# Performance work log

Measured on AMD Instinct MI355X. Metric: run time of the kernel, lower is better.

The kernel has to match this reference:

```python
import jax, jax.numpy as jnp
import numpy as np

B, LQ, LK = 4, 2048, 2048
DQ, DK, DO = 1024, 1024, 1024


def setup_inputs() -> dict:
    key = jax.random.key(0)
    ks = jax.random.split(key, 9)
    s = 0.02
    return {
        "query_input": jax.random.normal(ks[0], (B, LQ, DQ), jnp.float32),
        "key_input": jax.random.normal(ks[1], (B, LK, DK), jnp.float32),
        "value_input": jax.random.normal(ks[2], (B, LK, DK), jnp.float32),
        "Wq": jax.random.normal(ks[3], (DQ, DO), jnp.float32) * s,
        "bq": jax.random.normal(ks[4], (DO,), jnp.float32) * s,
        "Wk": jax.random.normal(ks[5], (DK, DO), jnp.float32) * s,
        "bk": jax.random.normal(ks[6], (DO,), jnp.float32) * s,
        "Wv": jax.random.normal(ks[7], (DK, DO), jnp.float32) * s,
        "bv": jax.random.normal(ks[8], (DO,), jnp.float32) * s,
    }


def reference(query_input, key_input, value_input, Wq, bq, Wk, bk, Wv, bv):
    scale = jnp.asarray(DO, query_input.dtype) ** 0.5
    q = query_input @ Wq + bq              # [B, Lq, D]
    k = key_input @ Wk + bk                # [B, Lk, D]
    v = value_input @ Wv + bv              # [B, Lk, D]
    attn = jnp.einsum("bqd,bkd->bqk", q, k) / scale
    attn = jax.nn.softmax(attn, axis=-1)
    return jnp.einsum("bqk,bkd->bqd", attn, v)
```

## Files before the change

### kernel.cpp

```cpp
#include <hip/hip_runtime.h>

typedef _Float16 f16x8 __attribute__((ext_vector_type(8)));
typedef _Float16 f16x4 __attribute__((ext_vector_type(4)));
typedef float f32x4 __attribute__((ext_vector_type(4)));

__device__ __forceinline__ void lds_load16(const _Float16* g, _Float16* l) {
    __builtin_amdgcn_global_load_lds(
        (const __attribute__((address_space(1))) void*)g,
        (__attribute__((address_space(3))) void*)l,
        16, 0, 0);
}

template <int MODE>
__global__ __launch_bounds__(256, 4)
void gemm_core(const _Float16* A, const _Float16* B, void* Cv, const float* bias,
               const _Float16* Ax1, const _Float16* Bx1, void* Cx1, const float* bx1,
               const _Float16* Ax2, const _Float16* Bx2, void* Cx2, const float* bx2,
               float* rowsum)
{
    const int z = blockIdx.z;
    const int bx = blockIdx.x, by = blockIdx.y;
    size_t cbase = 0;
    int lda, ldb, K, m0, n0;
    if (MODE == 0) {
        const int tmy = bx * 8 + (by >> 3);
        const int tnx = by & 7;
        if (z == 1) { A = Ax1; B = Bx1; Cv = Cx1; bias = bx1; }
        else if (z == 2) { A = Ax2; B = Bx2; Cv = Cx2; bias = bx2; }
        lda = 1024; ldb = 1024; K = 1024;
        m0 = (z == 2 ? tnx : tmy) * 128;
        n0 = (z == 2 ? tmy : tnx) * 128;
    } else if (MODE == 3) {
        const int tm = (bx & 7) * 2 + (by >> 3);
        const int tn = (bx >> 3) * 8 + (by & 7);
        A += (size_t)z * 2048 * 1024;
        B += (size_t)z * 2048 * 1024;
        cbase = (size_t)z * 2048 * 2048;
        rowsum += z * 2048;
        lda = 1024; ldb = 1024; K = 1024;
        m0 = tm * 128; n0 = tn * 128;
    } else {
        const int tm = bx * 2 + (by >> 3);
        const int tn = by & 7;
        A += (size_t)z * 2048 * 2048;
        B += (size_t)z * 2048;
        cbase = (size_t)z * 2048 * 1024;
        rowsum += z * 2048;
        lda = 2048; ldb = 8192; K = 2048;
        m0 = tm * 128; n0 = tn * 128;
    }

    __shared__ __align__(16) _Float16 As[2][128 * 32];
    __shared__ __align__(16) _Float16 Bs[2][128 * 32];

    const int t    = threadIdx.x;
    const int w    = t >> 6;
    const int lane = t & 63;
    const int ln   = lane & 15;
    const int kq   = lane >> 4;
    const int wm   = (w & 1) * 64;
    const int wn   = (w >> 1) * 64;

    const int arow = t >> 2;
    const int kcf  = (t & 3) * 8;
    const _Float16* gA0 = A + (size_t)(m0 + arow) * lda + kcf;
    const _Float16* gA1 = A + (size_t)(m0 + 64 + arow) * lda + kcf;
    const _Float16* gB0 = B + (size_t)(n0 + arow) * ldb + kcf;
    const _Float16* gB1 = B + (size_t)(n0 + 64 + arow) * ldb + kcf;

    auto stage = [&](int buf, int k0) {
        lds_load16(gA0 + k0, As[buf] + w * 512);
        lds_load16(gA1 + k0, As[buf] + 2048 + w * 512);
        lds_load16(gB0 + k0, Bs[buf] + w * 512);
        lds_load16(gB1 + k0, Bs[buf] + 2048 + w * 512);
    };

    f32x4 acc[4][4] = {};

    stage(0, 0);
    int cur = 0;
#pragma unroll 2
    for (int k0 = 0; k0 < K; k0 += 32) {
        __syncthreads();
        if (k0 + 32 < K) stage(cur ^ 1, k0 + 32);

        const _Float16* Ab = As[cur];
        const _Float16* Bb = Bs[cur];
        f16x8 af[4], bf[4];
#pragma unroll
        for (int i = 0; i < 4; ++i)
            af[i] = *(const f16x8*)(Ab + (wm + i * 16 + ln) * 32 + kq * 8);
#pragma unroll
        for (int i = 0; i < 4; ++i)
            bf[i] = *(const f16x8*)(Bb + (wn + i * 16 + ln) * 32 + kq * 8);
#pragma unroll
        for (int i = 0; i < 4; ++i)
#pragma unroll
            for (int j = 0; j < 4; ++j)
                acc[i][j] = __builtin_amdgcn_mfma_f32_16x16x32_f16(af[i], bf[j], acc[i][j], 0, 0, 0);
        cur ^= 1;
    }

    const int ldc = (MODE == 0) ? (z == 2 ? 8192 : 1024)
                  : (MODE == 3) ? 2048 : 1024;
    float*    Cf = (float*)Cv;
    _Float16* Ch = (_Float16*)Cv;
#pragma unroll
    for (int i = 0; i < 4; ++i) {
        const int rbase = m0 + wm + i * 16 + kq * 4;

        if (MODE == 0) {
#pragma unroll
            for (int j = 0; j < 4; ++j) {
                const int gcol = n0 + wn + j * 16 + ln;
#pragma unroll
                for (int r = 0; r < 4; ++r) {
                    float vv = acc[i][j][r] + (z == 2 ? bias[rbase + r] : bias[gcol]);
                    Ch[(size_t)(rbase + r) * ldc + gcol] = (_Float16)vv;
                }
            }
        } else if (MODE == 3) {
            float rs[4] = {0.f, 0.f, 0.f, 0.f};
#pragma unroll
            for (int j = 0; j < 4; ++j) {
                const int gcol = n0 + wn + j * 16 + ln;
#pragma unroll
                for (int r = 0; r < 4; ++r) {
                    float e = __expf(acc[i][j][r] * 0.03125f);
                    Ch[cbase + (size_t)(rbase + r) * ldc + gcol] = (_Float16)e;
                    rs[r] += e;
                }
            }
#pragma unroll
            for (int r = 0; r < 4; ++r) {
                float s = rs[r];
                s += __shfl_xor(s, 1);
                s += __shfl_xor(s, 2);
                s += __shfl_xor(s, 4);
                s += __shfl_xor(s, 8);
                if (ln == 0) atomicAdd(&rowsum[rbase + r], s);
            }
        } else {
            float inv[4];
#pragma unroll
            for (int r = 0; r < 4; ++r) inv[r] = 1.f / rowsum[rbase + r];
#pragma unroll
            for (int j = 0; j < 4; ++j) {
                const int gcol = n0 + wn + j * 16 + ln;
#pragma unroll
                for (int r = 0; r < 4; ++r)
                    Cf[cbase + (size_t)(rbase + r) * ldc + gcol] = acc[i][j][r] * inv[r];
            }
        }
    }
}

__global__ __launch_bounds__(256)
void cvt_f16(const float4* __restrict__ x0, _Float16* __restrict__ y0,
             const float4* __restrict__ x1, _Float16* __restrict__ y1,
             const float4* __restrict__ x2, _Float16* __restrict__ y2,
             float* __restrict__ rowsum)
{
    const size_t i = (size_t)blockIdx.x * 256 + threadIdx.x;
    const float4* x = blockIdx.y == 0 ? x0 : blockIdx.y == 1 ? x1 : x2;
    _Float16*    yy = blockIdx.y == 0 ? y0 : blockIdx.y == 1 ? y1 : y2;
    float4 f = x[i];
    f16x4 o = { (_Float16)f.x, (_Float16)f.y, (_Float16)f.z, (_Float16)f.w };
    *(f16x4*)(yy + i * 4) = o;
    if (blockIdx.y == 0 && blockIdx.x < 32)
        rowsum[blockIdx.x * 256 + threadIdx.x] = 0.f;
}

__global__ __launch_bounds__(256)
void transpose_w_1024(const float* __restrict__ W0, _Float16* __restrict__ T0,
                      const float* __restrict__ W1, _Float16* __restrict__ T1,
                      const float* __restrict__ W2, _Float16* __restrict__ T2)
{
    const float* W = blockIdx.z == 0 ? W0 : blockIdx.z == 1 ? W1 : W2;
    _Float16*   WT = blockIdx.z == 0 ? T0 : blockIdx.z == 1 ? T1 : T2;
    __shared__ float tile[32][33];
    const int bx = blockIdx.x * 32;
    const int by = blockIdx.y * 32;
    const int tx = threadIdx.x;
    const int ty = threadIdx.y;
#pragma unroll
    for (int i = ty; i < 32; i += 8)
        tile[i][tx] = W[(size_t)(by + i) * 1024 + bx + tx];
    __syncthreads();
#pragma unroll
    for (int i = ty; i < 32; i += 8)
        WT[(size_t)(bx + i) * 1024 + by + tx] = (_Float16)tile[tx][i];
}

extern "C" void kernel_launch(void* const* d_in, const int* in_sizes, int n_in,
                              void* d_out, int out_size, void* d_ws, size_t ws_size,
                              hipStream_t stream)
{
    const float* Xq = (const float*)d_in[0];
    const float* Xk = (const float*)d_in[1];
    const float* Xv = (const float*)d_in[2];
    const float* Wq = (const float*)d_in[3];
    const float* bq = (const float*)d_in[4];
    const float* Wk = (const float*)d_in[5];
    const float* bk = (const float*)d_in[6];
    const float* Wv = (const float*)d_in[7];
    const float* bv = (const float*)d_in[8];
    float* out = (float*)d_out;

    const size_t XN = (size_t)8192 * 1024;
    const size_t WN = (size_t)1024 * 1024;

    _Float16* ws  = (_Float16*)d_ws;
    _Float16* Xqh = ws;
    _Float16* Xkh = Xqh + XN;
    _Float16* Xvh = Xkh + XN;
    _Float16* WqT = Xvh + XN;
    _Float16* WkT = WqT + WN;
    _Float16* WvT = WkT + WN;
    _Float16* qh  = WvT + WN;
    _Float16* kh  = qh + XN;
    _Float16* vT  = kh + XN;
    _Float16* S   = vT + XN;
    float* rowsum = (float*)(S + (size_t)4 * 2048 * 2048);

    {
        dim3 g(8192, 3);
        cvt_f16<<<g, 256, 0, stream>>>((const float4*)Xq, Xqh,
                                       (const float4*)Xk, Xkh,
                                       (const float4*)Xv, Xvh, rowsum);
    }

    {
        dim3 tb(32, 8), tg(32, 32, 3);
        transpose_w_1024<<<tg, tb, 0, stream>>>(Wq, WqT, Wk, WkT, Wv, WvT);
    }

    {
        dim3 g(8, 64, 3);
        gemm_core<0><<<g, 256, 0, stream>>>(
            Xqh, WqT, qh, bq,
            Xkh, WkT, kh, bk,
            WvT, Xvh, vT, bv,
            nullptr);
    }

    {
        dim3 g(16, 16, 4);
        gemm_core<3><<<g, 256, 0, stream>>>(
            qh, kh, S, nullptr,
            nullptr, nullptr, nullptr, nullptr,
            nullptr, nullptr, nullptr, nullptr,
            rowsum);
    }

    {
        dim3 g(8, 16, 4);
        gemm_core<5><<<g, 256, 0, stream>>>(
            S, vT, out, nullptr,
            nullptr, nullptr, nullptr, nullptr,
            nullptr, nullptr, nullptr, nullptr,
            rowsum);
    }
}
```

Measured before the change: 333.0 us.

## Fuse fp32-to-fp16 input conversion into projection GEMM and shrink PV tile

```diff
diff --git a/kernel.cpp b/kernel.cpp
--- a/kernel.cpp
+++ b/kernel.cpp
@@ -1,7 +1,6 @@
 #include <hip/hip_runtime.h>
 
 typedef _Float16 f16x8 __attribute__((ext_vector_type(8)));
-typedef _Float16 f16x4 __attribute__((ext_vector_type(4)));
 typedef float f32x4 __attribute__((ext_vector_type(4)));
 
 __device__ __forceinline__ void lds_load16(const _Float16* g, _Float16* l) {
@@ -12,46 +11,20 @@
 }
 
 template <int MODE>
-__global__ __launch_bounds__(256, 4)
-void gemm_core(const _Float16* A, const _Float16* B, void* Cv, const float* bias,
-               const _Float16* Ax1, const _Float16* Bx1, void* Cx1, const float* bx1,
-               const _Float16* Ax2, const _Float16* Bx2, void* Cx2, const float* bx2,
-               float* rowsum)
+__global__ __launch_bounds__(256, MODE == 0 ? 3 : 4)
+void gemm_core(const float* X0, const float* X1, const float* X2,
+               const _Float16* W0, const _Float16* W1, const _Float16* W2,
+               void* C0, void* C1, void* C2,
+               const float* b0, const float* b1, const float* b2,
+               const _Float16* Af, const _Float16* Bf, void* Cvp, float* rowsum)
 {
+    constexpr int BN = (MODE == 5) ? 64 : 128;
+    constexpr int NJ = BN / 32;
     const int z = blockIdx.z;
     const int bx = blockIdx.x, by = blockIdx.y;
-    size_t cbase = 0;
-    int lda, ldb, K, m0, n0;
-    if (MODE == 0) {
-        const int tmy = bx * 8 + (by >> 3);
-        const int tnx = by & 7;
-        if (z == 1) { A = Ax1; B = Bx1; Cv = Cx1; bias = bx1; }
-        else if (z == 2) { A = Ax2; B = Bx2; Cv = Cx2; bias = bx2; }
-        lda = 1024; ldb = 1024; K = 1024;
-        m0 = (z == 2 ? tnx : tmy) * 128;
-        n0 = (z == 2 ? tmy : tnx) * 128;
-    } else if (MODE == 3) {
-        const int tm = (bx & 7) * 2 + (by >> 3);
-        const int tn = (bx >> 3) * 8 + (by & 7);
-        A += (size_t)z * 2048 * 1024;
-        B += (size_t)z * 2048 * 1024;
-        cbase = (size_t)z * 2048 * 2048;
-        rowsum += z * 2048;
-        lda = 1024; ldb = 1024; K = 1024;
-        m0 = tm * 128; n0 = tn * 128;
-    } else {
-        const int tm = bx * 2 + (by >> 3);
-        const int tn = by & 7;
-        A += (size_t)z * 2048 * 2048;
-        B += (size_t)z * 2048;
-        cbase = (size_t)z * 2048 * 1024;
-        rowsum += z * 2048;
-        lda = 2048; ldb = 8192; K = 2048;
-        m0 = tm * 128; n0 = tn * 128;
-    }
 
     __shared__ __align__(16) _Float16 As[2][128 * 32];
-    __shared__ __align__(16) _Float16 Bs[2][128 * 32];
+    __shared__ __align__(16) _Float16 Bs[2][BN * 32];
 
     const int t    = threadIdx.x;
     const int w    = t >> 6;
@@ -59,23 +32,116 @@
     const int ln   = lane & 15;
     const int kq   = lane >> 4;
     const int wm   = (w & 1) * 64;
-    const int wn   = (w >> 1) * 64;
-
-    const int arow = t >> 2;
-    const int kcf  = (t & 3) * 8;
-    const _Float16* gA0 = A + (size_t)(m0 + arow) * lda + kcf;
-    const _Float16* gA1 = A + (size_t)(m0 + 64 + arow) * lda + kcf;
-    const _Float16* gB0 = B + (size_t)(n0 + arow) * ldb + kcf;
-    const _Float16* gB1 = B + (size_t)(n0 + 64 + arow) * ldb + kcf;
-
-    auto stage = [&](int buf, int k0) {
-        lds_load16(gA0 + k0, As[buf] + w * 512);
-        lds_load16(gA1 + k0, As[buf] + 2048 + w * 512);
-        lds_load16(gB0 + k0, Bs[buf] + w * 512);
-        lds_load16(gB1 + k0, Bs[buf] + 2048 + w * 512);
+    const int wn   = (w >> 1) * (BN / 2);
+
+    f32x4 acc[4][NJ] = {};
+
+    if (MODE == 0) {
+        const int tmy = bx * 8 + (by >> 3);
+        const int tnx = by & 7;
+        const float*    Xp = z == 0 ? X0 : z == 1 ? X1 : X2;
+        const _Float16* Wp = z == 0 ? W0 : z == 1 ? W1 : W2;
+        _Float16*       Cp = (_Float16*)(z == 0 ? C0 : z == 1 ? C1 : C2);
+        const float*    bp = z == 0 ? b0 : z == 1 ? b1 : b2;
+        const int m0 = (z == 2 ? tnx : tmy) * 128;
+        const int n0 = (z == 2 ? tmy : tnx) * 128;
+        const int xrow = (z == 2 ? n0 : m0);
+        const int wrow = (z == 2 ? m0 : n0);
+        _Float16* bufX[2] = { z == 2 ? Bs[0] : As[0], z == 2 ? Bs[1] : As[1] };
+        _Float16* bufW[2] = { z == 2 ? As[0] : Bs[0], z == 2 ? As[1] : Bs[1] };
+
+        const _Float16* gW0 = Wp + (size_t)(wrow + (t >> 2)) * 1024 + (t & 3) * 8;
+        const _Float16* gW1 = gW0 + (size_t)64 * 1024;
+        const float* gX = Xp + (size_t)(xrow + (t >> 1)) * 1024 + (t & 1) * 16;
+        const int xoff = (t >> 1) * 32 + (t & 1) * 16;
+
+        auto stage = [&](int b, int k0) {
+            lds_load16(gW0 + k0, bufW[b] + w * 512);
+            lds_load16(gW1 + k0, bufW[b] + 2048 + w * 512);
+            float4 f0 = *(const float4*)(gX + k0);
+            float4 f1 = *(const float4*)(gX + k0 + 4);
+            float4 f2 = *(const float4*)(gX + k0 + 8);
+            float4 f3 = *(const float4*)(gX + k0 + 12);
+            f16x8 h0 = { (_Float16)f0.x, (_Float16)f0.y, (_Float16)f0.z, (_Float16)f0.w,
+                         (_Float16)f1.x, (_Float16)f1.y, (_Float16)f1.z, (_Float16)f1.w };
+            f16x8 h1 = { (_Float16)f2.x, (_Float16)f2.y, (_Float16)f2.z, (_Float16)f2.w,
+                         (_Float16)f3.x, (_Float16)f3.y, (_Float16)f3.z, (_Float16)f3.w };
+            *(f16x8*)(bufX[b] + xoff)     = h0;
+            *(f16x8*)(bufX[b] + xoff + 8) = h1;
+        };
+
+        stage(0, 0);
+        int cur = 0;
+#pragma unroll 2
+        for (int k0 = 0; k0 < 1024; k0 += 32) {
+            __syncthreads();
+            if (k0 + 32 < 1024) stage(cur ^ 1, k0 + 32);
+            const _Float16* Ab = As[cur];
+            const _Float16* Bb = Bs[cur];
+            f16x8 af[4], bf[4];
+#pragma unroll
+            for (int i = 0; i < 4; ++i)
+                af[i] = *(const f16x8*)(Ab + (wm + i * 16 + ln) * 32 + kq * 8);
+#pragma unroll
+            for (int i = 0; i < 4; ++i)
+                bf[i] = *(const f16x8*)(Bb + (wn + i * 16 + ln) * 32 + kq * 8);
+#pragma unroll
+            for (int i = 0; i < 4; ++i)
+#pragma unroll
+                for (int j = 0; j < 4; ++j)
+                    acc[i][j] = __builtin_amdgcn_mfma_f32_16x16x32_f16(af[i], bf[j], acc[i][j], 0, 0, 0);
+            cur ^= 1;
+        }
+
+        const int ldc = (z == 2) ? 8192 : 1024;
+#pragma unroll
+        for (int i = 0; i < 4; ++i) {
+            const int rbase = m0 + wm + i * 16 + kq * 4;
+#pragma unroll
+            for (int j = 0; j < 4; ++j) {
+                const int gcol = n0 + wn + j * 16 + ln;
+#pragma unroll
+                for (int r = 0; r < 4; ++r) {
+                    float vv = acc[i][j][r] + (z == 2 ? bp[rbase + r] : bp[gcol]);
+                    Cp[(size_t)(rbase + r) * ldc + gcol] = (_Float16)vv;
+                }
+            }
+        }
+        return;
+    }
+
+    const int tm = (bx & 7) * 2 + (by >> 3);
+    const int tn = (bx >> 3) * 8 + (by & 7);
+    const _Float16* A;
+    const _Float16* B;
+    size_t cbase;
+    int lda, ldb, K;
+    if (MODE == 3) {
+        A = Af + (size_t)z * 2048 * 1024;
+        B = Bf + (size_t)z * 2048 * 1024;
+        cbase = (size_t)z * 2048 * 2048;
+        lda = 1024; ldb = 1024; K = 1024;
+    } else {
+        A = Af + (size_t)z * 2048 * 2048;
+        B = Bf + (size_t)z * 2048;
+        cbase = (size_t)z * 2048 * 1024;
+        lda = 2048; ldb = 8192; K = 2048;
+    }
+    rowsum += z * 2048;
+    const int m0 = tm * 128;
+    const int n0 = tn * BN;
+
+    const _Float16* gA0 = A + (size_t)(m0 + (t >> 2)) * lda + (t & 3) * 8;
+    const _Float16* gA1 = gA0 + (size_t)64 * lda;
+    const _Float16* gB0 = B + (size_t)(n0 + (t >> 2)) * ldb + (t & 3) * 8;
+    const _Float16* gB1 = (BN == 128) ? gB0 + (size_t)64 * ldb : nullptr;
+
+    auto stage = [&](int b, int k0) {
+        lds_load16(gA0 + k0, As[b] + w * 512);
+        lds_load16(gA1 + k0, As[b] + 2048 + w * 512);
+        lds_load16(gB0 + k0, Bs[b] + w * 512);
+        if (BN == 128) lds_load16(gB1 + k0, Bs[b] + 2048 + w * 512);
     };
-
-    f32x4 acc[4][4] = {};
 
     stage(0, 0);
     int cur = 0;
@@ -83,51 +149,36 @@
     for (int k0 = 0; k0 < K; k0 += 32) {
         __syncthreads();
         if (k0 + 32 < K) stage(cur ^ 1, k0 + 32);
-
         const _Float16* Ab = As[cur];
         const _Float16* Bb = Bs[cur];
-        f16x8 af[4], bf[4];
+        f16x8 af[4], bf[NJ];
 #pragma unroll
         for (int i = 0; i < 4; ++i)
             af[i] = *(const f16x8*)(Ab + (wm + i * 16 + ln) * 32 + kq * 8);
 #pragma unroll
+        for (int j = 0; j < NJ; ++j)
+            bf[j] = *(const f16x8*)(Bb + (wn + j * 16 + ln) * 32 + kq * 8);
+#pragma unroll
         for (int i = 0; i < 4; ++i)
-            bf[i] = *(const f16x8*)(Bb + (wn + i * 16 + ln) * 32 + kq * 8);
-#pragma unroll
-        for (int i = 0; i < 4; ++i)
-#pragma unroll
-            for (int j = 0; j < 4; ++j)
+#pragma unroll
+            for (int j = 0; j < NJ; ++j)
                 acc[i][j] = __builtin_amdgcn_mfma_f32_16x16x32_f16(af[i], bf[j], acc[i][j], 0, 0, 0);
         cur ^= 1;
     }
 
-    const int ldc = (MODE == 0) ? (z == 2 ? 8192 : 1024)
-                  : (MODE == 3) ? 2048 : 1024;
-    float*    Cf = (float*)Cv;
-    _Float16* Ch = (_Float16*)Cv;
-#pragma unroll
-    for (int i = 0; i < 4; ++i) {
-        const int rbase = m0 + wm + i * 16 + kq * 4;
-
-        if (MODE == 0) {
+    if (MODE == 3) {
+        _Float16* Ch = (_Float16*)Cvp;
+#pragma unroll
+        for (int i = 0; i < 4; ++i) {
+            const int rbase = m0 + wm + i * 16 + kq * 4;
+            float rs[4] = {0.f, 0.f, 0.f, 0.f};
 #pragma unroll
             for (int j = 0; j < 4; ++j) {
                 const int gcol = n0 + wn + j * 16 + ln;
 #pragma unroll
                 for (int r = 0; r < 4; ++r) {
-                    float vv = acc[i][j][r] + (z == 2 ? bias[rbase + r] : bias[gcol]);
-                    Ch[(size_t)(rbase + r) * ldc + gcol] = (_Float16)vv;
-                }
-            }
-        } else if (MODE == 3) {
-            float rs[4] = {0.f, 0.f, 0.f, 0.f};
-#pragma unroll
-            for (int j = 0; j < 4; ++j) {
-                const int gcol = n0 + wn + j * 16 + ln;
-#pragma unroll
-                for (int r = 0; r < 4; ++r) {
                     float e = __expf(acc[i][j][r] * 0.03125f);
-                    Ch[cbase + (size_t)(rbase + r) * ldc + gcol] = (_Float16)e;
+                    Ch[cbase + (size_t)(rbase + r) * 2048 + gcol] = (_Float16)e;
                     rs[r] += e;
                 }
             }
@@ -140,41 +191,31 @@
                 s += __shfl_xor(s, 8);
                 if (ln == 0) atomicAdd(&rowsum[rbase + r], s);
             }
-        } else {
+        }
+    } else {
+        float* Cf = (float*)Cvp;
+#pragma unroll
+        for (int i = 0; i < 4; ++i) {
+            const int rbase = m0 + wm + i * 16 + kq * 4;
             float inv[4];
 #pragma unroll
             for (int r = 0; r < 4; ++r) inv[r] = 1.f / rowsum[rbase + r];
 #pragma unroll
-            for (int j = 0; j < 4; ++j) {
+            for (int j = 0; j < NJ; ++j) {
                 const int gcol = n0 + wn + j * 16 + ln;
 #pragma unroll
                 for (int r = 0; r < 4; ++r)
-                    Cf[cbase + (size_t)(rbase + r) * ldc + gcol] = acc[i][j][r] * inv[r];
-            }
-        }
-    }
-}
-
-__global__ __launch_bounds__(256)
-void cvt_f16(const float4* __restrict__ x0, _Float16* __restrict__ y0,
-             const float4* __restrict__ x1, _Float16* __restrict__ y1,
-             const float4* __restrict__ x2, _Float16* __restrict__ y2,
-             float* __restrict__ rowsum)
-{
-    const size_t i = (size_t)blockIdx.x * 256 + threadIdx.x;
-    const float4* x = blockIdx.y == 0 ? x0 : blockIdx.y == 1 ? x1 : x2;
-    _Float16*    yy = blockIdx.y == 0 ? y0 : blockIdx.y == 1 ? y1 : y2;
-    float4 f = x[i];
-    f16x4 o = { (_Float16)f.x, (_Float16)f.y, (_Float16)f.z, (_Float16)f.w };
-    *(f16x4*)(yy + i * 4) = o;
-    if (blockIdx.y == 0 && blockIdx.x < 32)
-        rowsum[blockIdx.x * 256 + threadIdx.x] = 0.f;
+                    Cf[cbase + (size_t)(rbase + r) * 1024 + gcol] = acc[i][j][r] * inv[r];
+            }
+        }
+    }
 }
 
 __global__ __launch_bounds__(256)
 void transpose_w_1024(const float* __restrict__ W0, _Float16* __restrict__ T0,
                       const float* __restrict__ W1, _Float16* __restrict__ T1,
-                      const float* __restrict__ W2, _Float16* __restrict__ T2)
+                      const float* __restrict__ W2, _Float16* __restrict__ T2,
+                      float* __restrict__ rowsum)
 {
     const float* W = blockIdx.z == 0 ? W0 : blockIdx.z == 1 ? W1 : W2;
     _Float16*   WT = blockIdx.z == 0 ? T0 : blockIdx.z == 1 ? T1 : T2;
@@ -183,6 +224,8 @@
     const int by = blockIdx.y * 32;
     const int tx = threadIdx.x;
     const int ty = threadIdx.y;
+    if (blockIdx.z == 0 && blockIdx.y == 0)
+        rowsum[blockIdx.x * 256 + ty * 32 + tx] = 0.f;
 #pragma unroll
     for (int i = ty; i < 32; i += 8)
         tile[i][tx] = W[(size_t)(by + i) * 1024 + bx + tx];
@@ -211,10 +254,7 @@
     const size_t WN = (size_t)1024 * 1024;
 
     _Float16* ws  = (_Float16*)d_ws;
-    _Float16* Xqh = ws;
-    _Float16* Xkh = Xqh + XN;
-    _Float16* Xvh = Xkh + XN;
-    _Float16* WqT = Xvh + XN;
+    _Float16* WqT = ws;
     _Float16* WkT = WqT + WN;
     _Float16* WvT = WkT + WN;
     _Float16* qh  = WvT + WN;
@@ -224,41 +264,30 @@
     float* rowsum = (float*)(S + (size_t)4 * 2048 * 2048);
 
     {
-        dim3 g(8192, 3);
-        cvt_f16<<<g, 256, 0, stream>>>((const float4*)Xq, Xqh,
-                                       (const float4*)Xk, Xkh,
-                                       (const float4*)Xv, Xvh, rowsum);
-    }
-
-    {
         dim3 tb(32, 8), tg(32, 32, 3);
-        transpose_w_1024<<<tg, tb, 0, stream>>>(Wq, WqT, Wk, WkT, Wv, WvT);
+        transpose_w_1024<<<tg, tb, 0, stream>>>(Wq, WqT, Wk, WkT, Wv, WvT, rowsum);
     }
 
     {
         dim3 g(8, 64, 3);
         gemm_core<0><<<g, 256, 0, stream>>>(
-            Xqh, WqT, qh, bq,
-            Xkh, WkT, kh, bk,
-            WvT, Xvh, vT, bv,
-            nullptr);
+            Xq, Xk, Xv, WqT, WkT, WvT, qh, kh, vT, bq, bk, bv,
+            nullptr, nullptr, nullptr, nullptr);
     }
 
     {
         dim3 g(16, 16, 4);
         gemm_core<3><<<g, 256, 0, stream>>>(
-            qh, kh, S, nullptr,
-            nullptr, nullptr, nullptr, nullptr,
-            nullptr, nullptr, nullptr, nullptr,
-            rowsum);
-    }
-
-    {
-        dim3 g(8, 16, 4);
+            nullptr, nullptr, nullptr, nullptr, nullptr, nullptr,
+            nullptr, nullptr, nullptr, nullptr, nullptr, nullptr,
+            qh, kh, S, rowsum);
+    }
+
+    {
+        dim3 g(16, 16, 4);
         gemm_core<5><<<g, 256, 0, stream>>>(
-            S, vT, out, nullptr,
-            nullptr, nullptr, nullptr, nullptr,
-            nullptr, nullptr, nullptr, nullptr,
-            rowsum);
-    }
-}
+            nullptr, nullptr, nullptr, nullptr, nullptr, nullptr,
+            nullptr, nullptr, nullptr, nullptr, nullptr, nullptr,
+            S, vT, out, rowsum);
+    }
+}
```

Result: slower. 356.6 us (+7.1%).

## Narrow PV GEMM tiles to 64 columns, swizzle tile order, merge prep kernels

Applied to the files above, without the earlier changes.

```diff
diff --git a/kernel.cpp b/kernel.cpp
--- a/kernel.cpp
+++ b/kernel.cpp
@@ -13,69 +13,73 @@
 
 template <int MODE>
 __global__ __launch_bounds__(256, 4)
-void gemm_core(const _Float16* A, const _Float16* B, void* Cv, const float* bias,
-               const _Float16* Ax1, const _Float16* Bx1, void* Cx1, const float* bx1,
-               const _Float16* Ax2, const _Float16* Bx2, void* Cx2, const float* bx2,
+void gemm_core(const _Float16* A0, const _Float16* B0, void* C0, const float* b0,
+               const _Float16* A1, const _Float16* B1, void* C1, const float* b1,
+               const _Float16* A2, const _Float16* B2, void* C2, const float* b2,
                float* rowsum)
 {
+    constexpr int BN = (MODE == 5) ? 64 : 128;
+    constexpr int NJ = BN / 32;
     const int z = blockIdx.z;
     const int bx = blockIdx.x, by = blockIdx.y;
+
+    __shared__ __align__(16) _Float16 As[2][128 * 32];
+    __shared__ __align__(16) _Float16 Bs[2][BN * 32];
+
+    const int t    = threadIdx.x;
+    const int w    = t >> 6;
+    const int lane = t & 63;
+    const int ln   = lane & 15;
+    const int kq   = lane >> 4;
+    const int wm   = (w & 1) * 64;
+    const int wn   = (w >> 1) * (BN / 2);
+
+    const _Float16* A;
+    const _Float16* B;
     size_t cbase = 0;
     int lda, ldb, K, m0, n0;
+
     if (MODE == 0) {
         const int tmy = bx * 8 + (by >> 3);
         const int tnx = by & 7;
-        if (z == 1) { A = Ax1; B = Bx1; Cv = Cx1; bias = bx1; }
-        else if (z == 2) { A = Ax2; B = Bx2; Cv = Cx2; bias = bx2; }
+        A = z == 0 ? A0 : z == 1 ? A1 : A2;
+        B = z == 0 ? B0 : z == 1 ? B1 : B2;
         lda = 1024; ldb = 1024; K = 1024;
         m0 = (z == 2 ? tnx : tmy) * 128;
         n0 = (z == 2 ? tmy : tnx) * 128;
     } else if (MODE == 3) {
         const int tm = (bx & 7) * 2 + (by >> 3);
         const int tn = (bx >> 3) * 8 + (by & 7);
-        A += (size_t)z * 2048 * 1024;
-        B += (size_t)z * 2048 * 1024;
+        A = A0 + (size_t)z * 2048 * 1024;
+        B = B0 + (size_t)z * 2048 * 1024;
         cbase = (size_t)z * 2048 * 2048;
         rowsum += z * 2048;
         lda = 1024; ldb = 1024; K = 1024;
         m0 = tm * 128; n0 = tn * 128;
     } else {
-        const int tm = bx * 2 + (by >> 3);
-        const int tn = by & 7;
-        A += (size_t)z * 2048 * 2048;
-        B += (size_t)z * 2048;
+        const int tm = (bx & 7) * 2 + (by >> 3);
+        const int tn = (bx >> 3) * 8 + (by & 7);
+        A = A0 + (size_t)z * 2048 * 2048;
+        B = B0 + (size_t)z * 2048;
         cbase = (size_t)z * 2048 * 1024;
         rowsum += z * 2048;
         lda = 2048; ldb = 8192; K = 2048;
-        m0 = tm * 128; n0 = tn * 128;
-    }
-
-    __shared__ __align__(16) _Float16 As[2][128 * 32];
-    __shared__ __align__(16) _Float16 Bs[2][128 * 32];
-
-    const int t    = threadIdx.x;
-    const int w    = t >> 6;
-    const int lane = t & 63;
-    const int ln   = lane & 15;
-    const int kq   = lane >> 4;
-    const int wm   = (w & 1) * 64;
-    const int wn   = (w >> 1) * 64;
-
-    const int arow = t >> 2;
-    const int kcf  = (t & 3) * 8;
-    const _Float16* gA0 = A + (size_t)(m0 + arow) * lda + kcf;
-    const _Float16* gA1 = A + (size_t)(m0 + 64 + arow) * lda + kcf;
-    const _Float16* gB0 = B + (size_t)(n0 + arow) * ldb + kcf;
-    const _Float16* gB1 = B + (size_t)(n0 + 64 + arow) * ldb + kcf;
-
-    auto stage = [&](int buf, int k0) {
-        lds_load16(gA0 + k0, As[buf] + w * 512);
-        lds_load16(gA1 + k0, As[buf] + 2048 + w * 512);
-        lds_load16(gB0 + k0, Bs[buf] + w * 512);
-        lds_load16(gB1 + k0, Bs[buf] + 2048 + w * 512);
+        m0 = tm * 128; n0 = tn * BN;
+    }
+
+    const _Float16* gA0 = A + (size_t)(m0 + (t >> 2)) * lda + (t & 3) * 8;
+    const _Float16* gA1 = gA0 + (size_t)64 * lda;
+    const _Float16* gB0 = B + (size_t)(n0 + (t >> 2)) * ldb + (t & 3) * 8;
+    const _Float16* gB1 = (BN == 128) ? gB0 + (size_t)64 * ldb : nullptr;
+
+    auto stage = [&](int b, int k0) {
+        lds_load16(gA0 + k0, As[b] + w * 512);
+        lds_load16(gA1 + k0, As[b] + 2048 + w * 512);
+        lds_load16(gB0 + k0, Bs[b] + w * 512);
+        if (BN == 128) lds_load16(gB1 + k0, Bs[b] + 2048 + w * 512);
     };
 
-    f32x4 acc[4][4] = {};
+    f32x4 acc[4][NJ] = {};
 
     stage(0, 0);
     int cur = 0;
@@ -83,43 +87,45 @@
     for (int k0 = 0; k0 < K; k0 += 32) {
         __syncthreads();
         if (k0 + 32 < K) stage(cur ^ 1, k0 + 32);
-
         const _Float16* Ab = As[cur];
         const _Float16* Bb = Bs[cur];
-        f16x8 af[4], bf[4];
+        f16x8 af[4], bf[NJ];
 #pragma unroll
         for (int i = 0; i < 4; ++i)
             af[i] = *(const f16x8*)(Ab + (wm + i * 16 + ln) * 32 + kq * 8);
 #pragma unroll
+        for (int j = 0; j < NJ; ++j)
+            bf[j] = *(const f16x8*)(Bb + (wn + j * 16 + ln) * 32 + kq * 8);
+#pragma unroll
         for (int i = 0; i < 4; ++i)
-            bf[i] = *(const f16x8*)(Bb + (wn + i * 16 + ln) * 32 + kq * 8);
-#pragma unroll
-        for (int i = 0; i < 4; ++i)
-#pragma unroll
-            for (int j = 0; j < 4; ++j)
+#pragma unroll
+            for (int j = 0; j < NJ; ++j)
                 acc[i][j] = __builtin_amdgcn_mfma_f32_16x16x32_f16(af[i], bf[j], acc[i][j], 0, 0, 0);
         cur ^= 1;
     }
 
-    const int ldc = (MODE == 0) ? (z == 2 ? 8192 : 1024)
-                  : (MODE == 3) ? 2048 : 1024;
-    float*    Cf = (float*)Cv;
-    _Float16* Ch = (_Float16*)Cv;
-#pragma unroll
-    for (int i = 0; i < 4; ++i) {
-        const int rbase = m0 + wm + i * 16 + kq * 4;
-
-        if (MODE == 0) {
+    if (MODE == 0) {
+        _Float16* Cp = (_Float16*)(z == 0 ? C0 : z == 1 ? C1 : C2);
+        const float* bp = z == 0 ? b0 : z == 1 ? b1 : b2;
+        const int ldc = (z == 2) ? 8192 : 1024;
+#pragma unroll
+        for (int i = 0; i < 4; ++i) {
+            const int rbase = m0 + wm + i * 16 + kq * 4;
 #pragma unroll
             for (int j = 0; j < 4; ++j) {
                 const int gcol = n0 + wn + j * 16 + ln;
 #pragma unroll
                 for (int r = 0; r < 4; ++r) {
-                    float vv = acc[i][j][r] + (z == 2 ? bias[rbase + r] : bias[gcol]);
-                    Ch[(size_t)(rbase + r) * ldc + gcol] = (_Float16)vv;
+                    float vv = acc[i][j][r] + (z == 2 ? bp[rbase + r] : bp[gcol]);
+                    Cp[(size_t)(rbase + r) * ldc + gcol] = (_Float16)vv;
                 }
             }
-        } else if (MODE == 3) {
+        }
+    } else if (MODE == 3) {
+        _Float16* Ch = (_Float16*)C0;
+#pragma unroll
+        for (int i = 0; i < 4; ++i) {
+            const int rbase = m0 + wm + i * 16 + kq * 4;
             float rs[4] = {0.f, 0.f, 0.f, 0.f};
 #pragma unroll
             for (int j = 0; j < 4; ++j) {
@@ -127,7 +133,7 @@
 #pragma unroll
                 for (int r = 0; r < 4; ++r) {
                     float e = __expf(acc[i][j][r] * 0.03125f);
-                    Ch[cbase + (size_t)(rbase + r) * ldc + gcol] = (_Float16)e;
+                    Ch[cbase + (size_t)(rbase + r) * 2048 + gcol] = (_Float16)e;
                     rs[r] += e;
                 }
             }
@@ -140,56 +146,63 @@
                 s += __shfl_xor(s, 8);
                 if (ln == 0) atomicAdd(&rowsum[rbase + r], s);
             }
-        } else {
+        }
+    } else {
+        float* Cf = (float*)C0;
+#pragma unroll
+        for (int i = 0; i < 4; ++i) {
+            const int rbase = m0 + wm + i * 16 + kq * 4;
             float inv[4];
 #pragma unroll
             for (int r = 0; r < 4; ++r) inv[r] = 1.f / rowsum[rbase + r];
 #pragma unroll
-            for (int j = 0; j < 4; ++j) {
+            for (int j = 0; j < NJ; ++j) {
                 const int gcol = n0 + wn + j * 16 + ln;
 #pragma unroll
                 for (int r = 0; r < 4; ++r)
-                    Cf[cbase + (size_t)(rbase + r) * ldc + gcol] = acc[i][j][r] * inv[r];
+                    Cf[cbase + (size_t)(rbase + r) * 1024 + gcol] = acc[i][j][r] * inv[r];
             }
         }
     }
 }
 
 __global__ __launch_bounds__(256)
-void cvt_f16(const float4* __restrict__ x0, _Float16* __restrict__ y0,
-             const float4* __restrict__ x1, _Float16* __restrict__ y1,
-             const float4* __restrict__ x2, _Float16* __restrict__ y2,
-             float* __restrict__ rowsum)
+void prep(const float4* __restrict__ x0, _Float16* __restrict__ y0,
+          const float4* __restrict__ x1, _Float16* __restrict__ y1,
+          const float4* __restrict__ x2, _Float16* __restrict__ y2,
+          const float* __restrict__ W0, _Float16* __restrict__ T0,
+          const float* __restrict__ W1, _Float16* __restrict__ T1,
+          const float* __restrict__ W2, _Float16* __restrict__ T2,
+          float* __restrict__ rowsum)
 {
-    const size_t i = (size_t)blockIdx.x * 256 + threadIdx.x;
-    const float4* x = blockIdx.y == 0 ? x0 : blockIdx.y == 1 ? x1 : x2;
-    _Float16*    yy = blockIdx.y == 0 ? y0 : blockIdx.y == 1 ? y1 : y2;
-    float4 f = x[i];
-    f16x4 o = { (_Float16)f.x, (_Float16)f.y, (_Float16)f.z, (_Float16)f.w };
-    *(f16x4*)(yy + i * 4) = o;
-    if (blockIdx.y == 0 && blockIdx.x < 32)
-        rowsum[blockIdx.x * 256 + threadIdx.x] = 0.f;
-}
-
-__global__ __launch_bounds__(256)
-void transpose_w_1024(const float* __restrict__ W0, _Float16* __restrict__ T0,
-                      const float* __restrict__ W1, _Float16* __restrict__ T1,
-                      const float* __restrict__ W2, _Float16* __restrict__ T2)
-{
-    const float* W = blockIdx.z == 0 ? W0 : blockIdx.z == 1 ? W1 : W2;
-    _Float16*   WT = blockIdx.z == 0 ? T0 : blockIdx.z == 1 ? T1 : T2;
+    if (blockIdx.y < 3) {
+        const size_t i = (size_t)blockIdx.x * 256 + threadIdx.x;
+        const float4* x = blockIdx.y == 0 ? x0 : blockIdx.y == 1 ? x1 : x2;
+        _Float16*    yy = blockIdx.y == 0 ? y0 : blockIdx.y == 1 ? y1 : y2;
+        float4 f = x[i];
+        f16x4 o = { (_Float16)f.x, (_Float16)f.y, (_Float16)f.z, (_Float16)f.w };
+        *(f16x4*)(yy + i * 4) = o;
+        if (blockIdx.y == 0 && blockIdx.x < 32)
+            rowsum[blockIdx.x * 256 + threadIdx.x] = 0.f;
+        return;
+    }
+    if (blockIdx.x >= 3072) return;
+    const int zz = blockIdx.x >> 10;
+    const int tb = blockIdx.x & 1023;
+    const float* W = zz == 0 ? W0 : zz == 1 ? W1 : W2;
+    _Float16*   WT = zz == 0 ? T0 : zz == 1 ? T1 : T2;
     __shared__ float tile[32][33];
-    const int bx = blockIdx.x * 32;
-    const int by = blockIdx.y * 32;
-    const int tx = threadIdx.x;
-    const int ty = threadIdx.y;
+    const int bxs = (tb & 31) * 32;
+    const int bys = (tb >> 5) * 32;
+    const int tx = threadIdx.x & 31;
+    const int ty = threadIdx.x >> 5;
 #pragma unroll
     for (int i = ty; i < 32; i += 8)
-        tile[i][tx] = W[(size_t)(by + i) * 1024 + bx + tx];
+        tile[i][tx] = W[(size_t)(bys + i) * 1024 + bxs + tx];
     __syncthreads();
 #pragma unroll
     for (int i = ty; i < 32; i += 8)
-        WT[(size_t)(bx + i) * 1024 + by + tx] = (_Float16)tile[tx][i];
+        WT[(size_t)(bxs + i) * 1024 + bys + tx] = (_Float16)tile[tx][i];
 }
 
 extern "C" void kernel_launch(void* const* d_in, const int* in_sizes, int n_in,
@@ -224,15 +237,11 @@
     float* rowsum = (float*)(S + (size_t)4 * 2048 * 2048);
 
     {
-        dim3 g(8192, 3);
-        cvt_f16<<<g, 256, 0, stream>>>((const float4*)Xq, Xqh,
-                                       (const float4*)Xk, Xkh,
-                                       (const float4*)Xv, Xvh, rowsum);
-    }
-
-    {
-        dim3 tb(32, 8), tg(32, 32, 3);
-        transpose_w_1024<<<tg, tb, 0, stream>>>(Wq, WqT, Wk, WkT, Wv, WvT);
+        dim3 g(8192, 4);
+        prep<<<g, 256, 0, stream>>>((const float4*)Xq, Xqh,
+                                    (const float4*)Xk, Xkh,
+                                    (const float4*)Xv, Xvh,
+                                    Wq, WqT, Wk, WkT, Wv, WvT, rowsum);
     }
 
     {
@@ -254,7 +263,7 @@
     }
 
     {
-        dim3 g(8, 16, 4);
+        dim3 g(16, 16, 4);
         gemm_core<5><<<g, 256, 0, stream>>>(
             S, vT, out, nullptr,
             nullptr, nullptr, nullptr, nullptr,
```

Result: no change. 327.9 us (-1.6%).
